# Kernel optimization log

Hardware: AMD Instinct MI355X
Metric: run time of the kernel (lower is better)

The kernel has to match this reference:

```python
import jax, jax.numpy as jnp
import numpy as np

HEADS = 6
WSIZE = 8
SHIFTS = 4
EPS = 1e-5


def conv1x1(x, w, b=None):
    # x: (B,C,H,W), w: (O,C)
    y = jnp.einsum('bchw,oc->bohw', x, w)
    if b is not None:
        y = y + b[None, :, None, None]
    return y


def spatial_shift(x):
    # ShiftConv2d1 depthwise fixed-kernel conv == per-group spatial shift with zero pad
    C = x.shape[1]
    g = C // 5
    x0, x1, x2, x3, x4 = (x[:, :g], x[:, g:2 * g], x[:, 2 * g:3 * g],
                          x[:, 3 * g:4 * g], x[:, 4 * g:])
    left = jnp.pad(x0[:, :, :, 1:], ((0, 0), (0, 0), (0, 0), (0, 1)))   # kernel (1,2)
    right = jnp.pad(x1[:, :, :, :-1], ((0, 0), (0, 0), (0, 0), (1, 0)))  # kernel (1,0)
    up = jnp.pad(x2[:, :, 1:, :], ((0, 0), (0, 0), (0, 1), (0, 0)))      # kernel (2,1)
    down = jnp.pad(x3[:, :, :-1, :], ((0, 0), (0, 0), (1, 0), (0, 0)))   # kernel (0,1)
    return jnp.concatenate([left, right, up, down, x4], axis=1)


def window_attn(xb, ws, heads, shifts):
    # xb: (B, 2*heads*c, H, W); self-similarity attention q@q^T (no separate K, no scaling)
    if shifts > 0:
        xb = jnp.roll(xb, (-(ws // 2), -(ws // 2)), axis=(2, 3))
    b, c2, H, W = xb.shape
    cd = c2 // (2 * heads)
    nh, nw = H // ws, W // ws
    t = xb.reshape(b, 2, heads, cd, nh, ws, nw, ws)
    t = t.transpose(1, 0, 4, 6, 2, 5, 7, 3).reshape(2, b * nh * nw, heads, ws * ws, cd)
    q, v = t[0], t[1]
    atn = jax.nn.softmax(jnp.einsum('whnc,whmc->whnm', q, q), axis=-1)
    o = jnp.einsum('whnm,whmc->whnc', atn, v)
    o = o.reshape(b, nh, nw, heads, ws, ws, cd)
    o = o.transpose(0, 3, 6, 1, 4, 2, 5).reshape(b, heads * cd, H, W)
    if shifts > 0:
        o = jnp.roll(o, (ws // 2, ws // 2), axis=(2, 3))
    return o


def setup_inputs() -> dict:
    key = jax.random.key(0)
    ks = jax.random.split(key, 8)
    B, C, H, W = 2, 180, 256, 256
    s = 0.05
    return {
        'x': jax.random.normal(ks[0], (B, C, H, W), jnp.float32),
        'w0': jax.random.normal(ks[1], (2 * C, C), jnp.float32) * s,
        'b0': jnp.zeros((2 * C,), jnp.float32),
        'w1': jax.random.normal(ks[2], (C, 2 * C), jnp.float32) * s,
        'b1': jnp.zeros((C,), jnp.float32),
        'w_in': jax.random.normal(ks[3], (2 * C, C), jnp.float32) * s,
        'b_in': jnp.zeros((2 * C,), jnp.float32),
        'bn_g': jnp.ones((2 * C,), jnp.float32),
        'bn_b': jnp.zeros((2 * C,), jnp.float32),
        'w_out': jax.random.normal(ks[4], (C, C), jnp.float32) * s,
        'b_out': jnp.zeros((C,), jnp.float32),
    }


def reference(x, w0, b0, w1, b1, w_in, b_in, bn_g, bn_b, w_out, b_out):
    # --- LFE (shift-conv FFN), exp_ratio=2, relu ---
    y = conv1x1(spatial_shift(x), w0, b0)
    y = jax.nn.relu(y)
    y = conv1x1(spatial_shift(y), w1, b1)
    x = y + x
    # --- GMSA (3 parallel shifted-window self-similarity attentions) ---
    z = conv1x1(x, w_in, b_in)
    mu = z.mean(axis=(0, 2, 3), keepdims=True)
    var = z.var(axis=(0, 2, 3), keepdims=True)  # biased, matching BN training forward
    z = (z - mu) / jnp.sqrt(var + EPS) * bn_g[None, :, None, None] + bn_b[None, :, None, None]
    cs = z.shape[1] // 3
    sizes = [WSIZE // 4, WSIZE // 2, WSIZE]
    outs = [window_attn(z[:, i * cs:(i + 1) * cs], sizes[i], HEADS, SHIFTS)
            for i in range(3)]
    out = conv1x1(jnp.concatenate(outs, axis=1), w_out, b_out)
    return out + x
```

## Files before the change

kernel.cpp:

```cpp
#include <hip/hip_runtime.h>
#include <hip/hip_bf16.h>

#define HWSZ 65536
#define NPIX 131072

typedef unsigned short u16;
typedef __bf16 bf16x8 __attribute__((ext_vector_type(8)));
typedef float f32x4 __attribute__((ext_vector_type(4)));
typedef unsigned short u16x2 __attribute__((ext_vector_type(2)));
typedef unsigned short u16x4 __attribute__((ext_vector_type(4)));
typedef unsigned short u16x8 __attribute__((ext_vector_type(8)));

__device__ inline u16 f2bf(float f) {
    unsigned int x = __builtin_bit_cast(unsigned int, f);
    unsigned int r = x + 0x7FFFu + ((x >> 16) & 1u);
    return (u16)(r >> 16);
}
__device__ inline float bf2f(u16 u) {
    unsigned int x = ((unsigned int)u) << 16;
    return __builtin_bit_cast(float, x);
}

__global__ __launch_bounds__(256) void prep_w(
    const float* __restrict__ w0, const float* __restrict__ w1,
    const float* __restrict__ wi, const float* __restrict__ wo,
    u16* __restrict__ W0p, u16* __restrict__ W1p,
    u16* __restrict__ Wip, u16* __restrict__ Wop)
{
    const int i = blockIdx.x * 256 + threadIdx.x;
    {
        const int r = i / 192, c = i % 192;
        const bool ok = (r < 360) && (c < 180);
        W0p[i] = ok ? f2bf(w0[r * 180 + c]) : (u16)0;
        Wip[i] = ok ? f2bf(wi[r * 180 + c]) : (u16)0;
    }
    {
        const int r = i / 384, c = i % 384;
        W1p[i] = (r < 180 && c < 360) ? f2bf(w1[r * 360 + c]) : (u16)0;
    }
    if (i < 36864) {
        const int r = i / 192, c = i % 192;
        Wop[i] = (r < 180 && c < 180) ? f2bf(wo[r * 180 + c]) : (u16)0;
    }
}

template<int CI, int CO, int G, int INM, int XSTR, bool RELU, int RES, int OUTM, int OSTR, bool COSPLIT>
__global__ __launch_bounds__(256, 4) void conv_v9(
    const void* __restrict__ Xv, const u16* __restrict__ Wp,
    const float* __restrict__ bias, const void* __restrict__ Rv,
    void* __restrict__ Yv)
{
    constexpr int CI_PAD = ((CI + 31) / 32) * 32;
    constexpr int NSTEP  = CI_PAD / 32;
    constexpr int LDK    = 40;

    __shared__ u16 Xt[2][64 * LDK];

    const int tid = threadIdx.x;
    const int bid = blockIdx.x;
    int px_tile, co0;
    if (COSPLIT) {
        co0     = ((bid >> 3) & 1) * 192;
        px_tile = ((bid >> 4) << 3) | (bid & 7);
    } else {
        co0 = 0; px_tile = bid;
    }
    const int p0   = px_tile << 6;
    const int b    = p0 >> 16;
    const int pix0 = p0 & 65535;
    const int h    = pix0 >> 8;
    const int w0c  = pix0 & 255;
    const int lane = tid & 63, wid = tid >> 6;
    const int lr = lane & 15, lg = lane >> 4;
    const int co_wave = co0 + wid * 48;

    const float* Xf = (const float*)Xv + (size_t)b * CI * HWSZ;
    const u16*   Xh = (const u16*)Xv;

    const int xn  = tid & 63;
    const int k4a = tid >> 6;

    auto loadX = [&](int kt, u16x4 (&r)[2]) {
        #pragma unroll
        for (int it = 0; it < 2; ++it) {
            const int k4 = k4a + it * 4;
            const int c0 = kt + k4 * 4;
            u16x4 v = {0, 0, 0, 0};
            if (c0 < CI) {
                int dh = 0, dw = 0;
                if (G > 0) {
                    const int g = c0 / G;
                    if      (g == 0) dw = 1;
                    else if (g == 1) dw = -1;
                    else if (g == 2) dh = 1;
                    else if (g == 3) dh = -1;
                }
                const int hh = h + dh;
                const int wp = w0c + xn + dw;
                if (hh >= 0 && hh < 256 && wp >= 0 && wp < 256) {
                    if constexpr (INM == 1) {
                        v = *(const u16x4*)&Xh[(size_t)((b << 16) | (hh << 8) | wp) * XSTR + c0];
                    } else {
                        const float* xs = Xf + (size_t)c0 * HWSZ + hh * 256 + wp;
                        #pragma unroll
                        for (int j = 0; j < 4; ++j) v[j] = f2bf(xs[(size_t)j * HWSZ]);
                    }
                }
            }
            r[it] = v;
        }
    };

    auto loadW = [&](int kt, bf16x8 (&a)[3]) {
        #pragma unroll
        for (int mf = 0; mf < 3; ++mf)
            a[mf] = *(const bf16x8*)&Wp[(size_t)(co_wave + mf * 16 + lr) * CI_PAD + kt + lg * 8];
    };

    auto writeLDS = [&](u16x4 (&r)[2], int buf) {
        *(u16x4*)&Xt[buf][xn * LDK + k4a * 4]       = r[0];
        *(u16x4*)&Xt[buf][xn * LDK + (k4a + 4) * 4] = r[1];
    };

    f32x4 acc[3][4] = {};
    u16x4 raw[2][2];
    bf16x8 af[2][3];

    loadX(0, raw[0]);
    loadW(0, af[0]);
    writeLDS(raw[0], 0);

    #pragma unroll
    for (int s = 0; s < NSTEP; ++s) {
        const int cur = s & 1, nxt = cur ^ 1;
        __syncthreads();
        if (s + 1 < NSTEP) {
            loadX((s + 1) * 32, raw[nxt]);
            loadW((s + 1) * 32, af[nxt]);
        }
        bf16x8 bfr[4];
        #pragma unroll
        for (int nf = 0; nf < 4; ++nf)
            bfr[nf] = *(const bf16x8*)&Xt[cur][(nf * 16 + lr) * LDK + lg * 8];
        #pragma unroll
        for (int mf = 0; mf < 3; ++mf)
            #pragma unroll
            for (int nf = 0; nf < 4; ++nf)
                acc[mf][nf] = __builtin_amdgcn_mfma_f32_16x16x32_bf16(
                    af[cur][mf], bfr[nf], acc[mf][nf], 0, 0, 0);
        if (s + 1 < NSTEP) writeLDS(raw[nxt], nxt);
    }

    const float* Rf = (const float*)Rv;
    const u16*   Rh = (const u16*)Rv;
    #pragma unroll
    for (int mf = 0; mf < 3; ++mf) {
        const int co_b = co_wave + mf * 16 + lg * 4;
        if (co_b >= CO) continue;
        #pragma unroll
        for (int nf = 0; nf < 4; ++nf) {
            const int pl = pix0 + nf * 16 + lr;
            const size_t pg = (size_t)p0 + nf * 16 + lr;
            float v[4];
            #pragma unroll
            for (int r = 0; r < 4; ++r) {
                v[r] = acc[mf][nf][r] + bias[co_b + r];
                if (RELU) v[r] = fmaxf(v[r], 0.f);
            }
            if (RES == 1) {
                #pragma unroll
                for (int r = 0; r < 4; ++r)
                    v[r] += Rf[((size_t)(b * CO + co_b + r)) * HWSZ + pl];
            }
            if (RES == 2) {
                u16x4 rr = *(const u16x4*)&Rh[pg * 180 + co_b];
                #pragma unroll
                for (int r = 0; r < 4; ++r) v[r] += bf2f(rr[r]);
            }
            if (OUTM == 1) {
                u16x4 o;
                #pragma unroll
                for (int r = 0; r < 4; ++r) o[r] = f2bf(v[r]);
                *(u16x4*)&((u16*)Yv)[pg * OSTR + co_b] = o;
            } else {
                #pragma unroll
                for (int r = 0; r < 4; ++r)
                    ((float*)Yv)[((size_t)(b * CO + co_b + r)) * HWSZ + pl] = v[r];
            }
        }
    }
}

__global__ __launch_bounds__(256) void bn_part(const u16* __restrict__ zt,
                                               float* __restrict__ part)
{
    const int tid = threadIdx.x;
    const int oc  = tid & 63;
    const int pp  = tid >> 6;
    if (oc >= 45) return;
    const int stripe = blockIdx.x * 4 + pp;
    const int pb = blockIdx.x * 1024 + pp;
    float s[8] = {}, q[8] = {};
    for (int i = 0; i < 256; ++i) {
        const int p = pb + i * 4;
        u16x8 t = *(const u16x8*)&zt[(size_t)p * 360 + oc * 8];
        #pragma unroll
        for (int j = 0; j < 8; ++j) {
            float v = bf2f(t[j]);
            s[j] += v; q[j] += v * v;
        }
    }
    float* pr = part + ((size_t)stripe * 45 + oc) * 16;
    #pragma unroll
    for (int j = 0; j < 8; ++j) { pr[j] = s[j]; pr[8 + j] = q[j]; }
}

__global__ __launch_bounds__(256) void bn_fin(const float* __restrict__ part,
                                              const float* __restrict__ g,
                                              const float* __restrict__ bb,
                                              float* __restrict__ sc,
                                              float* __restrict__ sh)
{
    const int oc = blockIdx.x;
    const int t  = threadIdx.x;
    const float* p1 = part + ((size_t)t * 45 + oc) * 16;
    const float* p2 = part + ((size_t)(t + 256) * 45 + oc) * 16;
    float v[16];
    #pragma unroll
    for (int k = 0; k < 16; ++k) v[k] = p1[k] + p2[k];
    #pragma unroll
    for (int k = 0; k < 16; ++k)
        for (int m = 32; m; m >>= 1) v[k] += __shfl_xor(v[k], m, 64);
    __shared__ float red[4][16];
    if ((t & 63) == 0) {
        #pragma unroll
        for (int k = 0; k < 16; ++k) red[t >> 6][k] = v[k];
    }
    __syncthreads();
    if (t == 0) {
        const float invN = 1.f / (float)NPIX;
        #pragma unroll
        for (int j = 0; j < 8; ++j) {
            const int c = oc * 8 + j;
            float su = red[0][j] + red[1][j] + red[2][j] + red[3][j];
            float sq = red[0][8+j] + red[1][8+j] + red[2][8+j] + red[3][8+j];
            float mean = su * invN;
            float var  = sq * invN - mean * mean;
            float istd = 1.f / sqrtf(var + 1e-5f);
            float s = g[c] * istd;
            sc[c] = s;
            sh[c] = bb[c] - mean * s;
        }
    }
}

template<int WS>
__global__ __launch_bounds__(256) void attn_v2(
    const u16* __restrict__ zt, const float* __restrict__ scale,
    const float* __restrict__ shiftc, u16* __restrict__ ot, int chunk)
{
    constexpr int NP  = WS * WS;
    constexpr int GPB = 256 / NP;
    constexpr int SH  = WS / 2;
    constexpr int NW  = 256 / WS;

    __shared__ float qs[256 * 12];
    __shared__ float vs[256 * 12];

    const int tid = threadIdx.x;
    const int lg  = tid / NP;
    const int n   = tid % NP;
    const int gidx = blockIdx.x * GPB + lg;

    const int head = gidx % 6;
    const int win  = gidx / 6;
    const int wcol = win % NW;
    const int tmp  = win / NW;
    const int wrow = tmp % NW;
    const int b    = tmp / NW;

    const int i = n / WS, j = n % WS;
    const int hh = (wrow * WS + i + SH) & 255;
    const int ww = (wcol * WS + j + SH) & 255;
    const size_t zrow = (size_t)((b << 16) | (hh << 8) | ww) * 360;

    const int cq = chunk * 120 + head * 10;
    const int cv = cq + 60;

    float q[10];
    float* qrow = &qs[tid * 12];
    float* vrow = &vs[tid * 12];
    #pragma unroll
    for (int c2 = 0; c2 < 5; ++c2) {
        u16x2 uq = *(const u16x2*)&zt[zrow + cq + c2 * 2];
        u16x2 uv = *(const u16x2*)&zt[zrow + cv + c2 * 2];
        float q0 = bf2f(uq[0]) * scale[cq + c2 * 2]     + shiftc[cq + c2 * 2];
        float q1 = bf2f(uq[1]) * scale[cq + c2 * 2 + 1] + shiftc[cq + c2 * 2 + 1];
        float v0 = bf2f(uv[0]) * scale[cv + c2 * 2]     + shiftc[cv + c2 * 2];
        float v1 = bf2f(uv[1]) * scale[cv + c2 * 2 + 1] + shiftc[cv + c2 * 2 + 1];
        q[c2 * 2] = q0; q[c2 * 2 + 1] = q1;
        qrow[c2 * 2] = q0; qrow[c2 * 2 + 1] = q1;
        vrow[c2 * 2] = v0; vrow[c2 * 2 + 1] = v1;
    }
    qrow[10] = 0.f; qrow[11] = 0.f;
    vrow[10] = 0.f; vrow[11] = 0.f;
    __syncthreads();

    const float* qg = &qs[(lg * NP) * 12];
    const float* vg = &vs[(lg * NP) * 12];

    float mx = -1e30f;
    for (int m = 0; m < NP; ++m) {
        f32x4 a0 = *(const f32x4*)&qg[m * 12];
        f32x4 a1 = *(const f32x4*)&qg[m * 12 + 4];
        f32x4 a2 = *(const f32x4*)&qg[m * 12 + 8];
        float d = q[0]*a0[0] + q[1]*a0[1] + q[2]*a0[2] + q[3]*a0[3]
                + q[4]*a1[0] + q[5]*a1[1] + q[6]*a1[2] + q[7]*a1[3]
                + q[8]*a2[0] + q[9]*a2[1];
        mx = fmaxf(mx, d);
    }
    float s = 0.f;
    float o[10] = {};
    for (int m = 0; m < NP; ++m) {
        f32x4 a0 = *(const f32x4*)&qg[m * 12];
        f32x4 a1 = *(const f32x4*)&qg[m * 12 + 4];
        f32x4 a2 = *(const f32x4*)&qg[m * 12 + 8];
        float d = q[0]*a0[0] + q[1]*a0[1] + q[2]*a0[2] + q[3]*a0[3]
                + q[4]*a1[0] + q[5]*a1[1] + q[6]*a1[2] + q[7]*a1[3]
                + q[8]*a2[0] + q[9]*a2[1];
        float e = __expf(d - mx);
        s += e;
        f32x4 b0 = *(const f32x4*)&vg[m * 12];
        f32x4 b1 = *(const f32x4*)&vg[m * 12 + 4];
        f32x4 b2 = *(const f32x4*)&vg[m * 12 + 8];
        o[0] += e * b0[0]; o[1] += e * b0[1]; o[2] += e * b0[2]; o[3] += e * b0[3];
        o[4] += e * b1[0]; o[5] += e * b1[1]; o[6] += e * b1[2]; o[7] += e * b1[3];
        o[8] += e * b2[0]; o[9] += e * b2[1];
    }
    const float inv = 1.f / s;
    u16* orow = ot + (size_t)((b << 16) | (hh << 8) | ww) * 180 + chunk * 60 + head * 10;
    #pragma unroll
    for (int c2 = 0; c2 < 5; ++c2) {
        u16x2 ov;
        ov[0] = f2bf(o[c2 * 2] * inv);
        ov[1] = f2bf(o[c2 * 2 + 1] * inv);
        *(u16x2*)&orow[c2 * 2] = ov;
    }
}

extern "C" void kernel_launch(void* const* d_in, const int* in_sizes, int n_in,
                              void* d_out, int out_size, void* d_ws, size_t ws_size,
                              hipStream_t stream)
{
    const float* x     = (const float*)d_in[0];
    const float* w0    = (const float*)d_in[1];
    const float* b0    = (const float*)d_in[2];
    const float* w1    = (const float*)d_in[3];
    const float* b1    = (const float*)d_in[4];
    const float* w_in  = (const float*)d_in[5];
    const float* b_in  = (const float*)d_in[6];
    const float* bn_g  = (const float*)d_in[7];
    const float* bn_b  = (const float*)d_in[8];
    const float* w_out = (const float*)d_in[9];
    const float* b_out = (const float*)d_in[10];
    float* out = (float*)d_out;

    u16* y   = (u16*)d_ws;
    u16* x1b = y   + (size_t)NPIX * 360;
    u16* ot  = x1b + (size_t)NPIX * 180;
    u16* W0p = ot  + (size_t)NPIX * 180;
    u16* Wip = W0p + 384 * 192;
    u16* W1p = Wip + 384 * 192;
    u16* Wop = W1p + 192 * 384;
    float* part   = (float*)(Wop + 192 * 192);
    float* scale  = part + 512 * 45 * 16;
    float* shiftc = scale + 360;
    u16* zt = y;

    dim3 blk(256);

    prep_w<<<dim3(288), blk, 0, stream>>>(w0, w1, w_in, w_out, W0p, W1p, Wip, Wop);

    conv_v9<180, 360, 36, 0, 0,   true,  0, 1, 360, true>
        <<<dim3(4096), blk, 0, stream>>>(x, W0p, b0, nullptr, y);
    conv_v9<360, 180, 72, 1, 360, false, 1, 1, 180, false>
        <<<dim3(2048), blk, 0, stream>>>(y, W1p, b1, x, x1b);
    conv_v9<180, 360, 0,  1, 180, false, 0, 1, 360, true>
        <<<dim3(4096), blk, 0, stream>>>(x1b, Wip, b_in, nullptr, zt);
    bn_part<<<dim3(128), blk, 0, stream>>>(zt, part);
    bn_fin<<<dim3(45), blk, 0, stream>>>(part, bn_g, bn_b, scale, shiftc);
    attn_v2<2><<<dim3(3072), blk, 0, stream>>>(zt, scale, shiftc, ot, 0);
    attn_v2<4><<<dim3(3072), blk, 0, stream>>>(zt, scale, shiftc, ot, 1);
    attn_v2<8><<<dim3(3072), blk, 0, stream>>>(zt, scale, shiftc, ot, 2);
    conv_v9<180, 180, 0,  1, 180, false, 2, 0, 0, false>
        <<<dim3(2048), blk, 0, stream>>>(ot, Wop, b_out, x1b, out);
}
```

Baseline: 424.5 us.

## Add double-buffered LDS conv kernel using async global-to-LDS loads for bf16 inputs

Adds a new 1x1 conv kernel for bf16 pixel-major inputs. Activation tiles are staged into double-buffered shared memory with global_load_lds direct copies, and the next K-step's weight fragments are prefetched in registers, so loads overlap the MFMA work. Channel order in LDS is swizzled by an XOR to avoid bank conflicts. It replaces the previous kernel for three of the four conv launches, with a scalar fallback path at group boundaries and image edges.

```diff
diff --git a/kernel.cpp b/kernel.cpp
--- a/kernel.cpp
+++ b/kernel.cpp
@@ -191,6 +191,161 @@
     }
 }
 
+template<int CI, int CO, int G, int XSTR, bool RELU, int RES, int OUTM, int OSTR, bool COSPLIT>
+__global__ __launch_bounds__(256) void conv_v10(
+    const u16* __restrict__ Xh, const u16* __restrict__ Wp,
+    const float* __restrict__ bias, const void* __restrict__ Rv,
+    void* __restrict__ Yv)
+{
+    constexpr int CI_PAD = ((CI + 31) / 32) * 32;
+    constexpr int NSTEP  = CI_PAD / 32;
+
+    __shared__ u16 Xt[2][256 * 8];
+
+    const int tid = threadIdx.x;
+    const int bid = blockIdx.x;
+    int px_tile, co0;
+    if (COSPLIT) {
+        co0     = ((bid >> 3) & 1) * 192;
+        px_tile = ((bid >> 4) << 3) | (bid & 7);
+    } else {
+        co0 = 0; px_tile = bid;
+    }
+    const int p0   = px_tile << 6;
+    const int b    = p0 >> 16;
+    const int pix0 = p0 & 65535;
+    const int h    = pix0 >> 8;
+    const int w0c  = pix0 & 255;
+    const int lane = tid & 63, wid = tid >> 6;
+    const int lr = lane & 15, lg = lane >> 4;
+    const int co_wave = co0 + wid * 48;
+
+    const int sg  = (wid << 6) | lane;
+    const int spx = sg >> 2;
+    const int khp = sg & 3;
+    const int kh  = khp ^ ((spx >> 1) & 3);
+
+    auto stage = [&](int kt, int buf) {
+        const int c0 = kt + kh * 8;
+        u16* ldst_lane = &Xt[buf][sg * 8];
+        int dh = 0, dw = 0; bool uni = true;
+        if (G > 0) {
+            const int g0 = c0 / G;
+            uni = (g0 == (c0 + 7) / G);
+            if      (g0 == 0) dw = 1;
+            else if (g0 == 1) dw = -1;
+            else if (g0 == 2) dh = 1;
+            else if (g0 == 3) dh = -1;
+        }
+        const int hh = h + dh, wp = w0c + spx + dw;
+        const bool pxok = (hh >= 0 && hh < 256 && wp >= 0 && wp < 256);
+        if (c0 < CI && uni && pxok) {
+            const u16* src = &Xh[(size_t)((b << 16) | (hh << 8) | wp) * XSTR + c0];
+            u16* wbase = &Xt[buf][(wid << 6) * 8];
+            __builtin_amdgcn_global_load_lds(
+                (const __attribute__((address_space(1))) unsigned int*)src,
+                (__attribute__((address_space(3))) unsigned int*)wbase, 16, 0, 0);
+        } else {
+            u16x8 t = {0, 0, 0, 0, 0, 0, 0, 0};
+            if (c0 < CI && pxok) {
+                #pragma unroll
+                for (int j = 0; j < 8; ++j) {
+                    const int c = c0 + j;
+                    if (c < CI) {
+                        int dh2 = 0, dw2 = 0;
+                        if (G > 0) {
+                            const int g = c / G;
+                            if      (g == 0) dw2 = 1;
+                            else if (g == 1) dw2 = -1;
+                            else if (g == 2) dh2 = 1;
+                            else if (g == 3) dh2 = -1;
+                        }
+                        const int h2 = h + dh2, w2 = w0c + spx + dw2;
+                        if (h2 >= 0 && h2 < 256 && w2 >= 0 && w2 < 256)
+                            t[j] = Xh[(size_t)((b << 16) | (h2 << 8) | w2) * XSTR + c];
+                    }
+                }
+            }
+            *(u16x8*)ldst_lane = t;
+        }
+    };
+
+    auto loadW = [&](int kt, bf16x8 (&a)[3]) {
+        #pragma unroll
+        for (int mf = 0; mf < 3; ++mf)
+            a[mf] = *(const bf16x8*)&Wp[(size_t)(co_wave + mf * 16 + lr) * CI_PAD + kt + lg * 8];
+    };
+
+    f32x4 acc[3][4] = {};
+    bf16x8 af[2][3];
+
+    stage(0, 0);
+    loadW(0, af[0]);
+    __syncthreads();
+
+    #pragma unroll
+    for (int s = 0; s < NSTEP; ++s) {
+        const int cur = s & 1, nxt = cur ^ 1;
+        if (s + 1 < NSTEP) {
+            stage((s + 1) * 32, nxt);
+            loadW((s + 1) * 32, af[nxt]);
+        }
+        bf16x8 bfr[4];
+        #pragma unroll
+        for (int nf = 0; nf < 4; ++nf) {
+            const int pxr = nf * 16 + lr;
+            const int kpp = lg ^ ((pxr >> 1) & 3);
+            bfr[nf] = *(const bf16x8*)&Xt[cur][pxr * 32 + kpp * 8];
+        }
+        #pragma unroll
+        for (int mf = 0; mf < 3; ++mf)
+            #pragma unroll
+            for (int nf = 0; nf < 4; ++nf)
+                acc[mf][nf] = __builtin_amdgcn_mfma_f32_16x16x32_bf16(
+                    af[cur][mf], bfr[nf], acc[mf][nf], 0, 0, 0);
+        __syncthreads();
+    }
+
+    const float* Rf = (const float*)Rv;
+    const u16*   Rh = (const u16*)Rv;
+    #pragma unroll
+    for (int mf = 0; mf < 3; ++mf) {
+        const int co_b = co_wave + mf * 16 + lg * 4;
+        if (co_b >= CO) continue;
+        #pragma unroll
+        for (int nf = 0; nf < 4; ++nf) {
+            const int pl = pix0 + nf * 16 + lr;
+            const size_t pg = (size_t)p0 + nf * 16 + lr;
+            float v[4];
+            #pragma unroll
+            for (int r = 0; r < 4; ++r) {
+                v[r] = acc[mf][nf][r] + bias[co_b + r];
+                if (RELU) v[r] = fmaxf(v[r], 0.f);
+            }
+            if (RES == 1) {
+                #pragma unroll
+                for (int r = 0; r < 4; ++r)
+                    v[r] += Rf[((size_t)(b * CO + co_b + r)) * HWSZ + pl];
+            }
+            if (RES == 2) {
+                u16x4 rr = *(const u16x4*)&Rh[pg * 180 + co_b];
+                #pragma unroll
+                for (int r = 0; r < 4; ++r) v[r] += bf2f(rr[r]);
+            }
+            if (OUTM == 1) {
+                u16x4 o;
+                #pragma unroll
+                for (int r = 0; r < 4; ++r) o[r] = f2bf(v[r]);
+                *(u16x4*)&((u16*)Yv)[pg * OSTR + co_b] = o;
+            } else {
+                #pragma unroll
+                for (int r = 0; r < 4; ++r)
+                    ((float*)Yv)[((size_t)(b * CO + co_b + r)) * HWSZ + pl] = v[r];
+            }
+        }
+    }
+}
+
 __global__ __launch_bounds__(256) void bn_part(const u16* __restrict__ zt,
                                                float* __restrict__ part)
 {
@@ -383,15 +538,15 @@
 
     conv_v9<180, 360, 36, 0, 0,   true,  0, 1, 360, true>
         <<<dim3(4096), blk, 0, stream>>>(x, W0p, b0, nullptr, y);
-    conv_v9<360, 180, 72, 1, 360, false, 1, 1, 180, false>
+    conv_v10<360, 180, 72, 360, false, 1, 1, 180, false>
         <<<dim3(2048), blk, 0, stream>>>(y, W1p, b1, x, x1b);
-    conv_v9<180, 360, 0,  1, 180, false, 0, 1, 360, true>
+    conv_v10<180, 360, 0,  180, false, 0, 1, 360, true>
         <<<dim3(4096), blk, 0, stream>>>(x1b, Wip, b_in, nullptr, zt);
     bn_part<<<dim3(128), blk, 0, stream>>>(zt, part);
     bn_fin<<<dim3(45), blk, 0, stream>>>(part, bn_g, bn_b, scale, shiftc);
     attn_v2<2><<<dim3(3072), blk, 0, stream>>>(zt, scale, shiftc, ot, 0);
     attn_v2<4><<<dim3(3072), blk, 0, stream>>>(zt, scale, shiftc, ot, 1);
     attn_v2<8><<<dim3(3072), blk, 0, stream>>>(zt, scale, shiftc, ot, 2);
-    conv_v9<180, 180, 0,  1, 180, false, 2, 0, 0, false>
+    conv_v10<180, 180, 0,  180, false, 2, 0, 0, false>
         <<<dim3(2048), blk, 0, stream>>>(ot, Wop, b_out, x1b, out);
 }
```

New measurement: 410.1 us. 1.04x faster.

## Convert input to NHWC bf16 and load conv fragments directly from global

Applied to the files above, without the earlier changes.

Adds a transpose kernel that converts the fp32 NCHW input into bf16 NHWC up front. All 1x1 convs then read their MFMA B fragments straight from global memory per lane, with no LDS staging, double buffering or block barriers. Spatial-shift groups are handled by per-pixel offsets, with a blend where a group boundary falls inside an 8-channel vector. This removes strided fp32 gathers and LDS sync costs, but adds an extra pass over the input. It also relies on unaligned vector global loads and uses a bf16 residual for the first block.

```diff
diff --git a/kernel.cpp b/kernel.cpp
--- a/kernel.cpp
+++ b/kernel.cpp
@@ -10,6 +10,7 @@
 typedef unsigned short u16x2 __attribute__((ext_vector_type(2)));
 typedef unsigned short u16x4 __attribute__((ext_vector_type(4)));
 typedef unsigned short u16x8 __attribute__((ext_vector_type(8)));
+typedef unsigned short u16x8u __attribute__((ext_vector_type(8), aligned(4)));
 
 __device__ inline u16 f2bf(float f) {
     unsigned int x = __builtin_bit_cast(unsigned int, f);
@@ -44,17 +45,41 @@
     }
 }
 
-template<int CI, int CO, int G, int INM, int XSTR, bool RELU, int RES, int OUTM, int OSTR, bool COSPLIT>
-__global__ __launch_bounds__(256, 4) void conv_v9(
-    const void* __restrict__ Xv, const u16* __restrict__ Wp,
+__global__ __launch_bounds__(256) void to_nhwc(const float* __restrict__ x,
+                                               u16* __restrict__ xb)
+{
+    __shared__ u16 T[64][188];
+    const int tid  = threadIdx.x;
+    const int p0   = blockIdx.x * 64;
+    const int b    = p0 >> 16;
+    const int pix0 = p0 & 65535;
+    const float* xsrc = x + (size_t)b * 180 * HWSZ + pix0;
+    #pragma unroll
+    for (int it = 0; it < 45; ++it) {
+        const int e  = it * 256 + tid;
+        const int c  = e >> 6, px = e & 63;
+        T[px][c] = f2bf(xsrc[(size_t)c * HWSZ + px]);
+    }
+    __syncthreads();
+    #pragma unroll
+    for (int it = 0; it < 12; ++it) {
+        const int e = it * 256 + tid;
+        if (e < 2880) {
+            const int px = e / 45, ci = e % 45;
+            *(u16x4*)&xb[(size_t)(p0 + px) * 180 + ci * 4] =
+                *(const u16x4*)&T[px][ci * 4];
+        }
+    }
+}
+
+template<int CI, int CO, int G, int XSTR, bool RELU, int RES, int OUTM, int OSTR, bool COSPLIT>
+__global__ __launch_bounds__(256) void conv_v11(
+    const u16* __restrict__ Xh, const u16* __restrict__ Wp,
     const float* __restrict__ bias, const void* __restrict__ Rv,
     void* __restrict__ Yv)
 {
     constexpr int CI_PAD = ((CI + 31) / 32) * 32;
     constexpr int NSTEP  = CI_PAD / 32;
-    constexpr int LDK    = 40;
-
-    __shared__ u16 Xt[2][64 * LDK];
 
     const int tid = threadIdx.x;
     const int bid = blockIdx.x;
@@ -68,87 +93,71 @@
     const int p0   = px_tile << 6;
     const int b    = p0 >> 16;
     const int pix0 = p0 & 65535;
-    const int h    = pix0 >> 8;
-    const int w0c  = pix0 & 255;
     const int lane = tid & 63, wid = tid >> 6;
     const int lr = lane & 15, lg = lane >> 4;
     const int co_wave = co0 + wid * 48;
 
-    const float* Xf = (const float*)Xv + (size_t)b * CI * HWSZ;
-    const u16*   Xh = (const u16*)Xv;
-
-    const int xn  = tid & 63;
-    const int k4a = tid >> 6;
-
-    auto loadX = [&](int kt, u16x4 (&r)[2]) {
-        #pragma unroll
-        for (int it = 0; it < 2; ++it) {
-            const int k4 = k4a + it * 4;
-            const int c0 = kt + k4 * 4;
-            u16x4 v = {0, 0, 0, 0};
-            if (c0 < CI) {
-                int dh = 0, dw = 0;
-                if (G > 0) {
-                    const int g = c0 / G;
-                    if      (g == 0) dw = 1;
-                    else if (g == 1) dw = -1;
-                    else if (g == 2) dh = 1;
-                    else if (g == 3) dh = -1;
+    int hhv[4], wpv[4];
+    long pbase[4];
+    #pragma unroll
+    for (int nf = 0; nf < 4; ++nf) {
+        const int pix = pix0 + nf * 16 + lr;
+        hhv[nf] = pix >> 8; wpv[nf] = pix & 255;
+        pbase[nf] = (long)((b << 16) | pix) * XSTR;
+    }
+
+    auto shiftOf = [&](int g, int nf, int& off, bool& ok) {
+        off = 0; ok = true;
+        if      (g == 0) { off =  XSTR;        ok = (wpv[nf] < 255); }
+        else if (g == 1) { off = -XSTR;        ok = (wpv[nf] > 0);   }
+        else if (g == 2) { off =  (XSTR << 8); ok = (hhv[nf] < 255); }
+        else if (g == 3) { off = -(XSTR << 8); ok = (hhv[nf] > 0);   }
+    };
+    auto loadv = [&](long idx) -> u16x8 {
+        return __builtin_bit_cast(u16x8, *(const u16x8u*)&Xh[idx]);
+    };
+
+    f32x4 acc[3][4] = {};
+
+    #pragma unroll
+    for (int s = 0; s < NSTEP; ++s) {
+        const int c0 = s * 32 + lg * 8;
+        bf16x8 bfr[4];
+        #pragma unroll
+        for (int nf = 0; nf < 4; ++nf) {
+            u16x8 a = {0, 0, 0, 0, 0, 0, 0, 0};
+            if constexpr (G > 0) {
+                const int g0 = (c0 < CI) ? (c0 / G) : 4;
+                int off0; bool ok0;
+                shiftOf(g0, nf, off0, ok0);
+                if (ok0) a = loadv(pbase[nf] + off0 + c0);
+                const int ce = (c0 + 7 < CI) ? (c0 + 7) : (CI - 1);
+                const int g1 = (c0 < CI) ? (ce / G) : 4;
+                if (g1 != g0) {
+                    int off1; bool ok1;
+                    shiftOf(g1, nf, off1, ok1);
+                    u16x8 b2 = {0, 0, 0, 0, 0, 0, 0, 0};
+                    if (ok1) b2 = loadv(pbase[nf] + off1 + c0);
+                    const int Bb = g1 * G;
+                    #pragma unroll
+                    for (int j = 0; j < 8; ++j)
+                        if (c0 + j >= Bb) a[j] = b2[j];
                 }
-                const int hh = h + dh;
-                const int wp = w0c + xn + dw;
-                if (hh >= 0 && hh < 256 && wp >= 0 && wp < 256) {
-                    if constexpr (INM == 1) {
-                        v = *(const u16x4*)&Xh[(size_t)((b << 16) | (hh << 8) | wp) * XSTR + c0];
-                    } else {
-                        const float* xs = Xf + (size_t)c0 * HWSZ + hh * 256 + wp;
-                        #pragma unroll
-                        for (int j = 0; j < 4; ++j) v[j] = f2bf(xs[(size_t)j * HWSZ]);
-                    }
-                }
+            } else {
+                a = loadv(pbase[nf] + c0);
             }
-            r[it] = v;
+            bfr[nf] = __builtin_bit_cast(bf16x8, a);
         }
-    };
-
-    auto loadW = [&](int kt, bf16x8 (&a)[3]) {
+        bf16x8 af[3];
         #pragma unroll
         for (int mf = 0; mf < 3; ++mf)
-            a[mf] = *(const bf16x8*)&Wp[(size_t)(co_wave + mf * 16 + lr) * CI_PAD + kt + lg * 8];
-    };
-
-    auto writeLDS = [&](u16x4 (&r)[2], int buf) {
-        *(u16x4*)&Xt[buf][xn * LDK + k4a * 4]       = r[0];
-        *(u16x4*)&Xt[buf][xn * LDK + (k4a + 4) * 4] = r[1];
-    };
-
-    f32x4 acc[3][4] = {};
-    u16x4 raw[2][2];
-    bf16x8 af[2][3];
-
-    loadX(0, raw[0]);
-    loadW(0, af[0]);
-    writeLDS(raw[0], 0);
-
-    #pragma unroll
-    for (int s = 0; s < NSTEP; ++s) {
-        const int cur = s & 1, nxt = cur ^ 1;
-        __syncthreads();
-        if (s + 1 < NSTEP) {
-            loadX((s + 1) * 32, raw[nxt]);
-            loadW((s + 1) * 32, af[nxt]);
-        }
-        bf16x8 bfr[4];
-        #pragma unroll
-        for (int nf = 0; nf < 4; ++nf)
-            bfr[nf] = *(const bf16x8*)&Xt[cur][(nf * 16 + lr) * LDK + lg * 8];
+            af[mf] = *(const bf16x8*)&Wp[(size_t)(co_wave + mf * 16 + lr) * CI_PAD + c0];
         #pragma unroll
         for (int mf = 0; mf < 3; ++mf)
             #pragma unroll
             for (int nf = 0; nf < 4; ++nf)
                 acc[mf][nf] = __builtin_amdgcn_mfma_f32_16x16x32_bf16(
-                    af[cur][mf], bfr[nf], acc[mf][nf], 0, 0, 0);
-        if (s + 1 < NSTEP) writeLDS(raw[nxt], nxt);
+                    af[mf], bfr[nf], acc[mf][nf], 0, 0, 0);
     }
 
     const float* Rf = (const float*)Rv;
@@ -375,23 +384,25 @@
     float* part   = (float*)(Wop + 192 * 192);
     float* scale  = part + 512 * 45 * 16;
     float* shiftc = scale + 360;
+    u16* xb = (u16*)(shiftc + 360);
     u16* zt = y;
 
     dim3 blk(256);
 
     prep_w<<<dim3(288), blk, 0, stream>>>(w0, w1, w_in, w_out, W0p, W1p, Wip, Wop);
-
-    conv_v9<180, 360, 36, 0, 0,   true,  0, 1, 360, true>
-        <<<dim3(4096), blk, 0, stream>>>(x, W0p, b0, nullptr, y);
-    conv_v9<360, 180, 72, 1, 360, false, 1, 1, 180, false>
-        <<<dim3(2048), blk, 0, stream>>>(y, W1p, b1, x, x1b);
-    conv_v9<180, 360, 0,  1, 180, false, 0, 1, 360, true>
+    to_nhwc<<<dim3(2048), blk, 0, stream>>>(x, xb);
+
+    conv_v11<180, 360, 36, 180, true,  0, 1, 360, true>
+        <<<dim3(4096), blk, 0, stream>>>(xb, W0p, b0, nullptr, y);
+    conv_v11<360, 180, 72, 360, false, 2, 1, 180, false>
+        <<<dim3(2048), blk, 0, stream>>>(y, W1p, b1, xb, x1b);
+    conv_v11<180, 360, 0,  180, false, 0, 1, 360, true>
         <<<dim3(4096), blk, 0, stream>>>(x1b, Wip, b_in, nullptr, zt);
     bn_part<<<dim3(128), blk, 0, stream>>>(zt, part);
     bn_fin<<<dim3(45), blk, 0, stream>>>(part, bn_g, bn_b, scale, shiftc);
     attn_v2<2><<<dim3(3072), blk, 0, stream>>>(zt, scale, shiftc, ot, 0);
     attn_v2<4><<<dim3(3072), blk, 0, stream>>>(zt, scale, shiftc, ot, 1);
     attn_v2<8><<<dim3(3072), blk, 0, stream>>>(zt, scale, shiftc, ot, 2);
-    conv_v9<180, 180, 0,  1, 180, false, 2, 0, 0, false>
+    conv_v11<180, 180, 0,  180, false, 2, 0, 0, false>
         <<<dim3(2048), blk, 0, stream>>>(ot, Wop, b_out, x1b, out);
 }
```

Result: slower. 445.6 us (+5.0%).
